# Optimization experiments

Hardware: AMD Instinct MI355X
Metric: run time of the kernel (lower is better)

The kernel has to match this reference:

```python
import jax, jax.numpy as jnp
import numpy as np

B, S, HID = 1, 1536, 6144
NH = 64           # num attention heads
DN = 128          # qk_nope_head_dim
DR = 64           # qk_rope_head_dim
DV = 128          # v_head_dim
QL = 1536         # q_lora_rank
KVL = 512         # kv_lora_rank
EPS = 1e-6
SM_SCALE = (DN + DR) ** -0.5            # qk_head_dim ** -0.5
SCALE_Q = (HID / QL) ** 0.5             # mla_scale_q_lora
SCALE_KV = (HID / KVL) ** 0.5           # mla_scale_kv_lora
ROPE_THETA = 10000.0


def rms_norm(x, w):
    xf = x.astype(jnp.float32)
    var = jnp.mean(xf * xf, axis=-1, keepdims=True)
    return (w * (xf * jax.lax.rsqrt(var + EPS))).astype(x.dtype)


def rotate_half(x):
    x1, x2 = jnp.split(x, 2, axis=-1)
    return jnp.concatenate([-x2, x1], axis=-1)


def setup_inputs() -> dict:
    key = jax.random.key(0)
    ks = jax.random.split(key, 8)
    hidden_states = jax.random.normal(ks[0], (B, S, HID), jnp.float32) * 0.02
    # rotary embeddings for the decoupled rope slice (dim DR)
    pos = jnp.arange(S, dtype=jnp.float32)
    inv_freq = 1.0 / (ROPE_THETA ** (jnp.arange(0, DR, 2, dtype=jnp.float32) / DR))
    freqs = pos[:, None] * inv_freq[None, :]          # [S, DR/2]
    emb = jnp.concatenate([freqs, freqs], axis=-1)    # [S, DR]
    cos, sin = jnp.cos(emb), jnp.sin(emb)
    w_qa = jax.random.normal(ks[1], (HID, QL), jnp.float32) / np.sqrt(HID)
    qa_ln_w = jnp.ones((QL,), jnp.float32)
    w_qb = jax.random.normal(ks[2], (QL, NH * (DN + DR)), jnp.float32) / np.sqrt(QL)
    w_kva = jax.random.normal(ks[3], (HID, KVL + DR), jnp.float32) / np.sqrt(HID)
    kva_ln_w = jnp.ones((KVL,), jnp.float32)
    # weight-absorbed kv_b_proj split: w_k [H, DN, KVL], w_v [H, KVL, DV]
    w_k = jax.random.normal(ks[4], (NH, DN, KVL), jnp.float32) / np.sqrt(KVL)
    w_v = jax.random.normal(ks[5], (NH, KVL, DV), jnp.float32) / np.sqrt(KVL)
    w_o = jax.random.normal(ks[6], (NH * DV, HID), jnp.float32) / np.sqrt(NH * DV)
    return {"hidden_states": hidden_states, "cos": cos, "sin": sin,
            "w_qa": w_qa, "qa_ln_w": qa_ln_w, "w_qb": w_qb,
            "w_kva": w_kva, "kva_ln_w": kva_ln_w,
            "w_k": w_k, "w_v": w_v, "w_o": w_o}


def reference(hidden_states, cos, sin, w_qa, qa_ln_w, w_qb, w_kva, kva_ln_w, w_k, w_v, w_o):
    b, s, _ = hidden_states.shape
    # --- Q path: low-rank compression + norm + scale + up-projection ---
    q_lat = rms_norm(hidden_states @ w_qa, qa_ln_w) * SCALE_Q        # [b,s,QL]
    q = (q_lat @ w_qb).reshape(b, s, NH, DN + DR)                    # [b,s,H,192]
    q_nope, q_pe = q[..., :DN], q[..., DN:]
    # --- KV path: compressed latent + decoupled rope key (MQA, 1 kv head) ---
    latent = hidden_states @ w_kva                                   # [b,s,KVL+DR]
    c_kv = rms_norm(latent[..., :KVL], kva_ln_w) * SCALE_KV          # [b,s,KVL]
    k_pe = latent[..., KVL:]                                         # [b,s,DR]
    # --- decoupled RoPE on rope slices only ---
    c4, s4 = cos[None, :, None, :], sin[None, :, None, :]
    q_pe = q_pe * c4 + rotate_half(q_pe) * s4                        # [b,s,H,DR]
    k_pe = k_pe * cos[None] + rotate_half(k_pe) * sin[None]          # [b,s,DR]
    # --- weight absorption: project q_nope into latent space via w_k ---
    q_abs = jnp.einsum('bshd,hdc->bshc', q_nope, w_k)                # [b,s,H,KVL]
    scores = (jnp.einsum('bshc,btc->bhst', q_abs, c_kv)
              + jnp.einsum('bshr,btr->bhst', q_pe, k_pe)) * SM_SCALE # [b,H,s,s]
    causal = jnp.tril(jnp.ones((s, s), bool))
    scores = jnp.where(causal[None, None], scores, jnp.finfo(scores.dtype).min)
    attn = jax.nn.softmax(scores, axis=-1)
    ctx = jnp.einsum('bhst,btc->bshc', attn, c_kv)                   # [b,s,H,KVL]
    out = jnp.einsum('bshc,hcd->bshd', ctx, w_v)                     # [b,s,H,DV]
    return out.reshape(b, s, NH * DV) @ w_o                          # [b,s,HID]
```

## Files before the change

### kernel.cpp

```cpp
#include <hip/hip_runtime.h>

using u16 = unsigned short;
typedef __bf16 bf16x8 __attribute__((ext_vector_type(8)));
typedef float f32x4 __attribute__((ext_vector_type(4)));

static constexpr int S = 1536;
static constexpr int HID = 6144;
static constexpr int NH = 64;
static constexpr int DN = 128;
static constexpr int DR = 64;
static constexpr int QL = 1536;
static constexpr int KVL = 512;
static constexpr float EPS = 1e-6f;
static constexpr float SM_SCALE = 0.07216878364870323f;
static constexpr float SCALE_Q = 2.0f;
static constexpr float SCALE_KV = 3.4641016151377544f;
static constexpr unsigned F32_ONE = 0x3F800000u;

__device__ inline float b2f(u16 x) {
    return __builtin_bit_cast(float, (unsigned)(((unsigned)x) << 16));
}
__device__ inline u16 f2b(float f) {
    __bf16 h = (__bf16)f;
    return __builtin_bit_cast(u16, h);
}
__device__ inline void storeC(float* p, float v) { *p = v; }
__device__ inline void storeC(u16* p, float v) { *p = f2b(v); }

typedef __attribute__((address_space(1))) void GV;
typedef __attribute__((address_space(3))) void LV;
__device__ inline void gload16(const u16* g, u16* l) {
    __builtin_amdgcn_global_load_lds((GV*)g, (LV*)l, 16, 0, 0);
}

__global__ __launch_bounds__(256)
void cvt_bf16(const void* __restrict__ src, u16* __restrict__ dst, long n,
              const unsigned* __restrict__ probe)
{
    const bool f32 = (*probe == F32_ONE);
    long i = ((long)blockIdx.x * 256 + threadIdx.x) * 8;
    if (i >= n) return;
    if (f32) {
        const float* s = (const float*)src + i;
        float4 a = *(const float4*)s;
        float4 b = *(const float4*)(s + 4);
        u16 t[8] = { f2b(a.x), f2b(a.y), f2b(a.z), f2b(a.w),
                     f2b(b.x), f2b(b.y), f2b(b.z), f2b(b.w) };
        *(uint4*)(dst + i) = *(uint4*)t;
    } else {
        *(uint4*)(dst + i) = *(const uint4*)((const u16*)src + i);
    }
}

__global__ __launch_bounds__(256)
void out_final(const u16* __restrict__ t, void* __restrict__ out, long n,
               const unsigned* __restrict__ probe)
{
    const bool f32 = (*probe == F32_ONE);
    long i = ((long)blockIdx.x * 256 + threadIdx.x) * 8;
    if (i >= n) return;
    uint4 v = *(const uint4*)(t + i);
    const u16* p = (const u16*)&v;
    if (f32) {
        float* o = (float*)out + i;
        #pragma unroll
        for (int j = 0; j < 8; ++j) o[j] = b2f(p[j]);
    } else {
        *(uint4*)((u16*)out + i) = v;
    }
}

__global__ __launch_bounds__(256)
void tconv(const void* __restrict__ src, long sBatch, int ldS,
           u16* __restrict__ dst, long dBatch, int ldD,
           const unsigned* __restrict__ probe)
{
    __shared__ u16 t[64][72];
    const bool f32 = (probe != nullptr) && (*probe == F32_ONE);
    const int r0 = blockIdx.y * 64;
    const int c0 = blockIdx.x * 64;
    const int tid = threadIdx.x;
    const int rr = tid >> 2;
    const int cc = (tid & 3) * 16;

    if (f32) {
        const float* s = (const float*)src + (long)blockIdx.z * sBatch
                       + (long)(r0 + rr) * ldS + (c0 + cc);
        u16 tmp[16];
        #pragma unroll
        for (int k = 0; k < 4; ++k) {
            float4 v = *(const float4*)(s + 4 * k);
            tmp[4*k+0] = f2b(v.x); tmp[4*k+1] = f2b(v.y);
            tmp[4*k+2] = f2b(v.z); tmp[4*k+3] = f2b(v.w);
        }
        *(uint4*)&t[rr][cc]     = *(uint4*)&tmp[0];
        *(uint4*)&t[rr][cc + 8] = *(uint4*)&tmp[8];
    } else {
        const u16* s = (const u16*)src + (long)blockIdx.z * sBatch
                     + (long)(r0 + rr) * ldS + (c0 + cc);
        *(uint4*)&t[rr][cc]     = *(const uint4*)s;
        *(uint4*)&t[rr][cc + 8] = *(const uint4*)(s + 8);
    }
    __syncthreads();
    u16 o[16];
    #pragma unroll
    for (int j = 0; j < 16; ++j) o[j] = t[cc + j][rr];
    u16* d = dst + (long)blockIdx.z * dBatch + (long)(c0 + rr) * ldD + (r0 + cc);
    *(uint4*)d       = *(uint4*)&o[0];
    *(uint4*)(d + 8) = *(uint4*)&o[8];
}

template <typename OutT>
__global__ __launch_bounds__(256)
void gemm_bt(const u16* __restrict__ A, long aB, int lda,
             const u16* __restrict__ B, long bB, int ldb,
             OutT* __restrict__ C, long cB, int ldc,
             int K, int Nvalid, int causal)
{
    const long m0 = (long)blockIdx.y * 128;
    const long n0 = (long)blockIdx.x * 128;
    if (causal == 1 && n0 >= m0 + 128) return;

    int Keff = K;
    if (causal == 2) { long kl = m0 + 128; Keff = (kl < K) ? (int)kl : K; }

    __shared__ __align__(16) u16 As[128 * 32];
    __shared__ __align__(16) u16 Bs[128 * 32];

    const int tid = threadIdx.x;
    const int lane = tid & 63, wave = tid >> 6;
    const int wm = wave >> 1, wn = wave & 1;
    const int quad = lane >> 4, r16 = lane & 15;

    A += (long)blockIdx.z * aB;
    B += (long)blockIdx.z * bB;
    C += (long)blockIdx.z * cB;

    const int srow = tid >> 2;
    const int scol = (tid & 3) * 8;

    const u16* aP  = A + (m0 + srow) * (long)lda + scol;
    const u16* aP2 = aP + 64 * (long)lda;
    const u16* bP  = B + (n0 + srow) * (long)ldb + scol;
    const u16* bP2 = bP + 64 * (long)ldb;
    u16* lA = As + srow * 32 + scol;
    u16* lB = Bs + srow * 32 + scol;

    f32x4 acc[4][4] = {};

    for (int k0 = 0; k0 < Keff; k0 += 32) {
        __syncthreads();
        gload16(aP  + k0, lA);
        gload16(aP2 + k0, lA + 64 * 32);
        gload16(bP  + k0, lB);
        gload16(bP2 + k0, lB + 64 * 32);
        asm volatile("s_waitcnt vmcnt(0)" ::: "memory");
        __syncthreads();

        bf16x8 af[4], bfr[4];
        #pragma unroll
        for (int i = 0; i < 4; ++i)
            af[i] = *(const bf16x8*)&As[(wm * 64 + i * 16 + r16) * 32 + quad * 8];
        #pragma unroll
        for (int j = 0; j < 4; ++j)
            bfr[j] = *(const bf16x8*)&Bs[(wn * 64 + j * 16 + r16) * 32 + quad * 8];
        #pragma unroll
        for (int i = 0; i < 4; ++i) {
            #pragma unroll
            for (int j = 0; j < 4; ++j)
                acc[i][j] = __builtin_amdgcn_mfma_f32_16x16x32_bf16(af[i], bfr[j], acc[i][j], 0, 0, 0);
        }
    }

    #pragma unroll
    for (int i = 0; i < 4; ++i) {
        long r = m0 + wm * 64 + i * 16 + quad * 4;
        #pragma unroll
        for (int j = 0; j < 4; ++j) {
            int c = (int)n0 + wn * 64 + j * 16 + r16;
            if (c < Nvalid) {
                #pragma unroll
                for (int g = 0; g < 4; ++g)
                    storeC(&C[(r + g) * (long)ldc + c], acc[i][j][g]);
            }
        }
    }
}

__global__ __launch_bounds__(256)
void gemm_bt_sk(const u16* __restrict__ A, int lda,
                const u16* __restrict__ B, int ldb,
                float* __restrict__ C, long cPlane, int ldc,
                int kSeg, int Nvalid)
{
    const long m0 = (long)blockIdx.y * 128;
    const long n0 = (long)blockIdx.x * 128;
    const long kBase = (long)blockIdx.z * kSeg;

    __shared__ __align__(16) u16 As[128 * 32];
    __shared__ __align__(16) u16 Bs[128 * 32];

    const int tid = threadIdx.x;
    const int lane = tid & 63, wave = tid >> 6;
    const int wm = wave >> 1, wn = wave & 1;
    const int quad = lane >> 4, r16 = lane & 15;

    const int srow = tid >> 2;
    const int scol = (tid & 3) * 8;

    const u16* aP  = A + (m0 + srow) * (long)lda + kBase + scol;
    const u16* aP2 = aP + 64 * (long)lda;
    const u16* bP  = B + (n0 + srow) * (long)ldb + kBase + scol;
    const u16* bP2 = bP + 64 * (long)ldb;
    u16* lA = As + srow * 32 + scol;
    u16* lB = Bs + srow * 32 + scol;

    f32x4 acc[4][4] = {};

    for (int k0 = 0; k0 < kSeg; k0 += 32) {
        __syncthreads();
        gload16(aP  + k0, lA);
        gload16(aP2 + k0, lA + 64 * 32);
        gload16(bP  + k0, lB);
        gload16(bP2 + k0, lB + 64 * 32);
        asm volatile("s_waitcnt vmcnt(0)" ::: "memory");
        __syncthreads();

        bf16x8 af[4], bfr[4];
        #pragma unroll
        for (int i = 0; i < 4; ++i)
            af[i] = *(const bf16x8*)&As[(wm * 64 + i * 16 + r16) * 32 + quad * 8];
        #pragma unroll
        for (int j = 0; j < 4; ++j)
            bfr[j] = *(const bf16x8*)&Bs[(wn * 64 + j * 16 + r16) * 32 + quad * 8];
        #pragma unroll
        for (int i = 0; i < 4; ++i) {
            #pragma unroll
            for (int j = 0; j < 4; ++j)
                acc[i][j] = __builtin_amdgcn_mfma_f32_16x16x32_bf16(af[i], bfr[j], acc[i][j], 0, 0, 0);
        }
    }

    float* Cz = C + (long)blockIdx.z * cPlane;
    #pragma unroll
    for (int i = 0; i < 4; ++i) {
        long r = m0 + wm * 64 + i * 16 + quad * 4;
        #pragma unroll
        for (int j = 0; j < 4; ++j) {
            int c = (int)n0 + wn * 64 + j * 16 + r16;
            if (c < Nvalid) {
                #pragma unroll
                for (int g = 0; g < 4; ++g)
                    Cz[(r + g) * (long)ldc + c] = acc[i][j][g];
            }
        }
    }
}

__global__ __launch_bounds__(256)
void sk_reduce(const float* __restrict__ parts, long n, long plane, int nsplit,
               void* __restrict__ out, int mode, const unsigned* __restrict__ probe)
{
    long i = ((long)blockIdx.x * 256 + threadIdx.x) * 4;
    if (i >= n) return;
    float4 s = *(const float4*)(parts + i);
    for (int p = 1; p < nsplit; ++p) {
        float4 v = *(const float4*)(parts + (long)p * plane + i);
        s.x += v.x; s.y += v.y; s.z += v.z; s.w += v.w;
    }
    const bool f32o = (mode == 0) || (*probe == F32_ONE);
    if (f32o) {
        *(float4*)((float*)out + i) = s;
    } else {
        u16 t[4] = { f2b(s.x), f2b(s.y), f2b(s.z), f2b(s.w) };
        *(uint2*)((u16*)out + i) = *(uint2*)t;
    }
}

__device__ inline float blockReduce(float v, bool isMax) {
    __shared__ float tmp[4];
    #pragma unroll
    for (int o = 32; o > 0; o >>= 1) {
        float ov = __shfl_down(v, o, 64);
        v = isMax ? fmaxf(v, ov) : v + ov;
    }
    int lane = threadIdx.x & 63, w = threadIdx.x >> 6;
    __syncthreads();
    if (lane == 0) tmp[w] = v;
    __syncthreads();
    v = tmp[0];
    #pragma unroll
    for (int i = 1; i < 4; ++i) v = isMax ? fmaxf(v, tmp[i]) : v + tmp[i];
    return v;
}

__global__ __launch_bounds__(256)
void qa_norm(const float* __restrict__ x, const u16* __restrict__ w, u16* __restrict__ out)
{
    int s = blockIdx.x;
    const float* row = x + (long)s * QL;
    float ss = 0.f;
    for (int c = threadIdx.x; c < QL; c += 256) { float v = row[c]; ss += v * v; }
    ss = blockReduce(ss, false);
    float inv = rsqrtf(ss / QL + EPS) * SCALE_Q;
    for (int c = threadIdx.x; c < QL; c += 256)
        out[(long)s * QL + c] = f2b(b2f(w[c]) * row[c] * inv);
}

__global__ __launch_bounds__(256)
void kva_norm_rope(const float* __restrict__ latent, const u16* __restrict__ w,
                   const u16* __restrict__ cosb, const u16* __restrict__ sinb,
                   u16* __restrict__ ckv)
{
    int s = blockIdx.x;
    const float* row = latent + (long)s * 576;
    float ss = 0.f;
    for (int c = threadIdx.x; c < KVL; c += 256) { float v = row[c]; ss += v * v; }
    ss = blockReduce(ss, false);
    float inv = rsqrtf(ss / KVL + EPS) * SCALE_KV;
    for (int c = threadIdx.x; c < KVL; c += 256)
        ckv[(long)s * 576 + c] = f2b(b2f(w[c]) * row[c] * inv);
    if (threadIdx.x < 64) {
        int d = threadIdx.x;
        float x = row[KVL + d];
        float other = (d < 32) ? -row[KVL + d + 32] : row[KVL + d - 32];
        float cv = b2f(cosb[s * 64 + d]), sv = b2f(sinb[s * 64 + d]);
        ckv[(long)s * 576 + KVL + d] = f2b(x * cv + other * sv);
    }
}

__global__ void rope_q(const u16* __restrict__ q, const u16* __restrict__ cosb,
                       const u16* __restrict__ sinb, u16* __restrict__ qcat, int h0)
{
    int s = blockIdx.x, z = blockIdx.y, d = threadIdx.x;
    const u16* qp = q + (long)s * 12288 + (h0 + z) * 192 + 128;
    float x = b2f(qp[d]);
    float other = (d < 32) ? -b2f(qp[d + 32]) : b2f(qp[d - 32]);
    float cv = b2f(cosb[s * 64 + d]), sv = b2f(sinb[s * 64 + d]);
    qcat[(long)z * (S * 576) + (long)s * 576 + 512 + d] = f2b(x * cv + other * sv);
}

__global__ __launch_bounds__(256)
void softmax_causal(float* __restrict__ scores)
{
    int s = blockIdx.x, z = blockIdx.y;
    float* row = scores + (long)z * S * S + (long)s * S;
    u16* prow = (u16*)row;
    int n = s + 1;
    float vloc[6];
    float m = -1e30f;
    #pragma unroll
    for (int i = 0; i < 6; ++i) {
        int t = threadIdx.x + i * 256;
        float v = (t < n) ? row[t] * SM_SCALE : -1e30f;
        vloc[i] = v;
        m = fmaxf(m, v);
    }
    m = blockReduce(m, true);
    float l = 0.f;
    #pragma unroll
    for (int i = 0; i < 6; ++i) {
        int t = threadIdx.x + i * 256;
        float e = (t < n) ? __expf(vloc[i] - m) : 0.f;
        vloc[i] = e;
        l += e;
    }
    l = blockReduce(l, false);
    float rinv = 1.f / l;
    #pragma unroll
    for (int i = 0; i < 6; ++i) {
        int t = threadIdx.x + i * 256;
        prow[t] = f2b(vloc[i] * rinv);
    }
}

extern "C" void kernel_launch(void* const* d_in, const int* in_sizes, int n_in,
                              void* d_out, int out_size, void* d_ws, size_t ws_size,
                              hipStream_t stream)
{
    (void)in_sizes; (void)n_in; (void)out_size;
    const unsigned* probe = (const unsigned*)d_in[4];

    const long nHid = (long)S * HID, nCos = (long)S * 64;
    const long nWqa = (long)HID * QL, nQln = QL;
    const long nWqb = (long)QL * 12288, nKln = KVL;
    const long nWk = (long)NH * DN * KVL, nWv = (long)NH * KVL * DN;
    const long nWo = (long)NH * DN * HID;

    char* ws = (char*)d_ws;
    size_t off = 0;
    auto a16 = [&](long n) { u16* p = (u16*)(ws + off); off += (size_t)n * 2; return p; };
    auto a32 = [&](long n) { float* p = (float*)(ws + off); off += (size_t)n * 4; return p; };

    u16* hid_b  = a16(nHid);
    u16* cos_b  = a16(nCos);
    u16* sin_b  = a16(nCos);
    u16* wqaT   = a16(nWqa);
    u16* qln_b  = a16(nQln);
    u16* wqbT   = a16(nWqb);
    u16* wkvaT  = a16(640L * HID);
    u16* kln_b  = a16(nKln);
    u16* wkT    = a16(nWk);
    u16* wvT    = a16(nWv);
    u16* woT    = a16(nWo);
    u16* ckvT   = a16((long)KVL * S);

    float* qlatr = a32((long)S * QL);
    float* latent = qlatr;
    u16* q_lat   = a16((long)S * QL);
    u16* qbuf    = a16((long)S * 12288);
    u16* ckv     = a16((long)S * 576);
    u16* ctxv    = a16((long)S * 8192);

    const size_t ctxAllB = (size_t)NH * S * KVL * 2;
    const size_t skOutB  = 2ul * (size_t)S * HID * 4;
    auto chunkB = [](int c) {
        return (size_t)c * S * 576 * 2 + (size_t)c * S * S * 4;
    };
    int C = 0;
    const int cand[4] = { 8, 4, 2, 1 };
    for (int ci = 0; ci < 4; ++ci) {
        size_t R = chunkB(cand[ci]); if (R < skOutB) R = skOutB;
        if (off + ctxAllB + R <= ws_size) { C = cand[ci]; break; }
    }

    auto cvt = [&](const void* s, u16* d, long n) {
        cvt_bf16<<<dim3((unsigned)((n / 8 + 255) / 256)), 256, 0, stream>>>(s, d, n, probe);
    };
    cvt(d_in[0], hid_b, nHid);
    cvt(d_in[1], cos_b, nCos);
    cvt(d_in[2], sin_b, nCos);
    cvt(d_in[4], qln_b, nQln);
    cvt(d_in[7], kln_b, nKln);

    tconv<<<dim3(24, 96, 1), 256, 0, stream>>>(d_in[3], 0, QL, wqaT, 0, HID, probe);
    tconv<<<dim3(192, 24, 1), 256, 0, stream>>>(d_in[5], 0, 12288, wqbT, 0, QL, probe);
    tconv<<<dim3(9, 96, 1), 256, 0, stream>>>(d_in[6], 0, 576, wkvaT, 0, HID, probe);
    tconv<<<dim3(8, 2, NH), 256, 0, stream>>>(d_in[8], (long)DN * KVL, KVL, wkT, (long)DN * KVL, DN, probe);
    tconv<<<dim3(2, 8, NH), 256, 0, stream>>>(d_in[9], (long)DN * KVL, DN, wvT, (long)DN * KVL, KVL, probe);
    tconv<<<dim3(96, 128, 1), 256, 0, stream>>>(d_in[10], 0, HID, woT, 0, 8192, probe);

    if (C > 0) {
        u16* ctxAll = a16((long)NH * S * KVL);
        char* Rbase = ws + off;
        float* skP   = (float*)Rbase;
        u16* qcat    = (u16*)Rbase;
        float* scores = (float*)(Rbase + (size_t)C * S * 576 * 2);

        auto rgrid = [](long n) { return dim3((unsigned)((n / 4 + 255) / 256)); };

        gemm_bt_sk<<<dim3(12, 12, 4), 256, 0, stream>>>(hid_b, HID, wqaT, HID,
                                                        skP, (long)S * QL, QL, HID / 4, QL);
        sk_reduce<<<rgrid((long)S * QL), 256, 0, stream>>>(skP, (long)S * QL, (long)S * QL, 4,
                                                           qlatr, 0, probe);
        qa_norm<<<S, 256, 0, stream>>>(qlatr, qln_b, q_lat);
        gemm_bt<u16><<<dim3(96, 12, 1), 256, 0, stream>>>(q_lat, 0, QL, wqbT, 0, QL,
                                                          qbuf, 0, 12288, QL, 12288, 0);
        gemm_bt_sk<<<dim3(5, 12, 8), 256, 0, stream>>>(hid_b, HID, wkvaT, HID,
                                                       skP, (long)S * 576, 576, HID / 8, 576);
        sk_reduce<<<rgrid((long)S * 576), 256, 0, stream>>>(skP, (long)S * 576, (long)S * 576, 8,
                                                            latent, 0, probe);
        kva_norm_rope<<<S, 256, 0, stream>>>(latent, kln_b, cos_b, sin_b, ckv);
        tconv<<<dim3(8, 24, 1), 256, 0, stream>>>(ckv, 0, 576, ckvT, 0, S, nullptr);

        for (int ch = 0; ch < NH / C; ++ch) {
            int h0 = ch * C;
            gemm_bt<u16><<<dim3(4, 12, C), 256, 0, stream>>>(
                qbuf + h0 * 192, 192, 12288, wkT + (size_t)h0 * 65536, 65536, DN,
                qcat, (long)S * 576, 576, DN, KVL, 0);
            rope_q<<<dim3(S, C), 64, 0, stream>>>(qbuf, cos_b, sin_b, qcat, h0);
            gemm_bt<float><<<dim3(12, 12, C), 256, 0, stream>>>(
                qcat, (long)S * 576, 576, ckv, 0, 576,
                scores, (long)S * S, S, 576, S, 1);
            softmax_causal<<<dim3(S, C), 256, 0, stream>>>(scores);
            gemm_bt<u16><<<dim3(4, 12, C), 256, 0, stream>>>(
                (const u16*)scores, (long)S * S * 2, 3072, ckvT, 0, S,
                ctxAll + (size_t)h0 * S * KVL, (long)S * KVL, KVL, S, KVL, 2);
        }
        gemm_bt<u16><<<dim3(1, 12, NH), 256, 0, stream>>>(
            ctxAll, (long)S * KVL, KVL, wvT, 65536, KVL,
            ctxv, 128, 8192, KVL, DN, 0);
        gemm_bt_sk<<<dim3(48, 12, 2), 256, 0, stream>>>(ctxv, 8192, woT, 8192,
                                                        skP, (long)S * HID, HID, 8192 / 2, HID);
        sk_reduce<<<rgrid(nHid), 256, 0, stream>>>(skP, nHid, nHid, 2, d_out, 2, probe);
    } else {
        const size_t perHB = (size_t)S * 576 * 2 + (size_t)S * S * 4 + (size_t)S * KVL * 2;
        int Cf = 1;
        if      (off + 8 * perHB <= ws_size) Cf = 8;
        else if (off + 4 * perHB <= ws_size) Cf = 4;
        else if (off + 2 * perHB <= ws_size) Cf = 2;

        u16* qcat    = a16((long)Cf * S * 576);
        float* scores = a32((long)Cf * S * S);
        u16* ctx     = a16((long)Cf * S * KVL);
        u16* outTmp  = wqaT;

        gemm_bt<float><<<dim3(12, 12, 1), 256, 0, stream>>>(hid_b, 0, HID, wqaT, 0, HID,
                                                            qlatr, 0, QL, HID, QL, 0);
        qa_norm<<<S, 256, 0, stream>>>(qlatr, qln_b, q_lat);
        gemm_bt<u16><<<dim3(96, 12, 1), 256, 0, stream>>>(q_lat, 0, QL, wqbT, 0, QL,
                                                          qbuf, 0, 12288, QL, 12288, 0);
        gemm_bt<float><<<dim3(5, 12, 1), 256, 0, stream>>>(hid_b, 0, HID, wkvaT, 0, HID,
                                                           latent, 0, 576, HID, 576, 0);
        kva_norm_rope<<<S, 256, 0, stream>>>(latent, kln_b, cos_b, sin_b, ckv);
        tconv<<<dim3(8, 24, 1), 256, 0, stream>>>(ckv, 0, 576, ckvT, 0, S, nullptr);

        for (int ch = 0; ch < NH / Cf; ++ch) {
            int h0 = ch * Cf;
            gemm_bt<u16><<<dim3(4, 12, Cf), 256, 0, stream>>>(
                qbuf + h0 * 192, 192, 12288, wkT + (size_t)h0 * 65536, 65536, DN,
                qcat, (long)S * 576, 576, DN, KVL, 0);
            rope_q<<<dim3(S, Cf), 64, 0, stream>>>(qbuf, cos_b, sin_b, qcat, h0);
            gemm_bt<float><<<dim3(12, 12, Cf), 256, 0, stream>>>(
                qcat, (long)S * 576, 576, ckv, 0, 576,
                scores, (long)S * S, S, 576, S, 1);
            softmax_causal<<<dim3(S, Cf), 256, 0, stream>>>(scores);
            gemm_bt<u16><<<dim3(4, 12, Cf), 256, 0, stream>>>(
                (const u16*)scores, (long)S * S * 2, 3072, ckvT, 0, S,
                ctx, (long)S * KVL, KVL, S, KVL, 2);
            gemm_bt<u16><<<dim3(1, 12, Cf), 256, 0, stream>>>(
                ctx, (long)S * KVL, KVL, wvT + (size_t)h0 * 65536, 65536, KVL,
                ctxv + h0 * 128, 128, 8192, KVL, DN, 0);
        }
        gemm_bt<u16><<<dim3(48, 12, 1), 256, 0, stream>>>(ctxv, 0, 8192, woT, 0, 8192,
                                                          outTmp, 0, HID, 8192, HID, 0);
        out_final<<<dim3((unsigned)((nHid / 8 + 255) / 256)), 256, 0, stream>>>(
            outTmp, d_out, nHid, probe);
    }
}
```

Before: 1.820 ms.

## Double GEMM K-tile with XOR-swizzled LDS, XCD-aware block remap, larger head chunks

Both GEMM kernels now stage a 64-wide K slice per iteration instead of 32, and run two MFMA sub-steps per barrier pair. Global loads are XOR-swizzled into the LDS rows to avoid bank conflicts on the fragment reads. A new xcd_remap reorders workgroups so that neighbouring output tiles land on the same XCD, for better L2 reuse; it is enabled for the large projection GEMMs and always for split-K. The attention head-chunk candidates now go up to 64 heads when the workspace allows, cutting launch count. The cost is twice the LDS per block and more index arithmetic, which may lower occupancy.

```diff
diff --git a/kernel.cpp b/kernel.cpp
--- a/kernel.cpp
+++ b/kernel.cpp
@@ -110,65 +110,85 @@
     *(uint4*)(d + 8) = *(uint4*)&o[8];
 }
 
+__device__ inline void xcd_remap(int& bx, int& by, int gx, int gy)
+{
+    const int nwg = gx * gy;
+    const int L = by * gx + bx;
+    const int q = nwg >> 3, r = nwg & 7;
+    const int xcd = L & 7, i = L >> 3;
+    const int d = ((xcd < r) ? xcd * (q + 1) : r * (q + 1) + (xcd - r) * q) + i;
+    bx = d / gy;  by = d - bx * gy;
+}
+
 template <typename OutT>
 __global__ __launch_bounds__(256)
 void gemm_bt(const u16* __restrict__ A, long aB, int lda,
              const u16* __restrict__ B, long bB, int ldb,
              OutT* __restrict__ C, long cB, int ldc,
-             int K, int Nvalid, int causal)
-{
-    const long m0 = (long)blockIdx.y * 128;
-    const long n0 = (long)blockIdx.x * 128;
+             int K, int Nvalid, int causal, int swz)
+{
+    int bx = blockIdx.x, by = blockIdx.y;
+    if (swz) xcd_remap(bx, by, gridDim.x, gridDim.y);
+    const long m0 = (long)by * 128;
+    const long n0 = (long)bx * 128;
     if (causal == 1 && n0 >= m0 + 128) return;
 
     int Keff = K;
     if (causal == 2) { long kl = m0 + 128; Keff = (kl < K) ? (int)kl : K; }
 
-    __shared__ __align__(16) u16 As[128 * 32];
-    __shared__ __align__(16) u16 Bs[128 * 32];
+    __shared__ __align__(16) u16 As[128 * 64];
+    __shared__ __align__(16) u16 Bs[128 * 64];
 
     const int tid = threadIdx.x;
     const int lane = tid & 63, wave = tid >> 6;
     const int wm = wave >> 1, wn = wave & 1;
     const int quad = lane >> 4, r16 = lane & 15;
+    const int rx = r16 & 7;
 
     A += (long)blockIdx.z * aB;
     B += (long)blockIdx.z * bB;
     C += (long)blockIdx.z * cB;
 
-    const int srow = tid >> 2;
-    const int scol = (tid & 3) * 8;
-
-    const u16* aP  = A + (m0 + srow) * (long)lda + scol;
-    const u16* aP2 = aP + 64 * (long)lda;
-    const u16* bP  = B + (n0 + srow) * (long)ldb + scol;
-    const u16* bP2 = bP + 64 * (long)ldb;
-    u16* lA = As + srow * 32 + scol;
-    u16* lB = Bs + srow * 32 + scol;
+    const int srow = tid >> 3;
+    const int gck = ((tid & 7) ^ (srow & 7)) * 8;
+
+    const u16* aP = A + (m0 + srow) * (long)lda + gck;
+    const u16* bP = B + (n0 + srow) * (long)ldb + gck;
+    u16* lA = As + tid * 8;
+    u16* lB = Bs + tid * 8;
+    const long l32a = 32 * (long)lda, l32b = 32 * (long)ldb;
 
     f32x4 acc[4][4] = {};
 
-    for (int k0 = 0; k0 < Keff; k0 += 32) {
+    for (int k0 = 0; k0 < Keff; k0 += 64) {
         __syncthreads();
-        gload16(aP  + k0, lA);
-        gload16(aP2 + k0, lA + 64 * 32);
-        gload16(bP  + k0, lB);
-        gload16(bP2 + k0, lB + 64 * 32);
+        gload16(aP + k0,            lA);
+        gload16(aP + l32a + k0,     lA + 2048);
+        gload16(aP + 2 * l32a + k0, lA + 4096);
+        gload16(aP + 3 * l32a + k0, lA + 6144);
+        gload16(bP + k0,            lB);
+        gload16(bP + l32b + k0,     lB + 2048);
+        gload16(bP + 2 * l32b + k0, lB + 4096);
+        gload16(bP + 3 * l32b + k0, lB + 6144);
         asm volatile("s_waitcnt vmcnt(0)" ::: "memory");
         __syncthreads();
 
-        bf16x8 af[4], bfr[4];
         #pragma unroll
-        for (int i = 0; i < 4; ++i)
-            af[i] = *(const bf16x8*)&As[(wm * 64 + i * 16 + r16) * 32 + quad * 8];
-        #pragma unroll
-        for (int j = 0; j < 4; ++j)
-            bfr[j] = *(const bf16x8*)&Bs[(wn * 64 + j * 16 + r16) * 32 + quad * 8];
-        #pragma unroll
-        for (int i = 0; i < 4; ++i) {
+        for (int kk = 0; kk < 2; ++kk) {
+            bf16x8 af[4], bfr[4];
+            const int ck = ((kk * 4 + quad) ^ rx) * 8;
+            #pragma unroll
+            for (int i = 0; i < 4; ++i)
+                af[i] = *(const bf16x8*)&As[(wm * 64 + i * 16 + r16) * 64 + ck];
             #pragma unroll
             for (int j = 0; j < 4; ++j)
-                acc[i][j] = __builtin_amdgcn_mfma_f32_16x16x32_bf16(af[i], bfr[j], acc[i][j], 0, 0, 0);
+                bfr[j] = *(const bf16x8*)&Bs[(wn * 64 + j * 16 + r16) * 64 + ck];
+            #pragma unroll
+            for (int i = 0; i < 4; ++i) {
+                #pragma unroll
+                for (int j = 0; j < 4; ++j)
+                    acc[i][j] = __builtin_amdgcn_mfma_f32_16x16x32_bf16(af[i], bfr[j], acc[i][j], 0, 0, 0);
+            }
         }
     }
 
@@ -193,51 +213,61 @@
                 float* __restrict__ C, long cPlane, int ldc,
                 int kSeg, int Nvalid)
 {
-    const long m0 = (long)blockIdx.y * 128;
-    const long n0 = (long)blockIdx.x * 128;
+    int bx = blockIdx.x, by = blockIdx.y;
+    xcd_remap(bx, by, gridDim.x, gridDim.y);
+    const long m0 = (long)by * 128;
+    const long n0 = (long)bx * 128;
     const long kBase = (long)blockIdx.z * kSeg;
 
-    __shared__ __align__(16) u16 As[128 * 32];
-    __shared__ __align__(16) u16 Bs[128 * 32];
+    __shared__ __align__(16) u16 As[128 * 64];
+    __shared__ __align__(16) u16 Bs[128 * 64];
 
     const int tid = threadIdx.x;
     const int lane = tid & 63, wave = tid >> 6;
     const int wm = wave >> 1, wn = wave & 1;
     const int quad = lane >> 4, r16 = lane & 15;
-
-    const int srow = tid >> 2;
-    const int scol = (tid & 3) * 8;
-
-    const u16* aP  = A + (m0 + srow) * (long)lda + kBase + scol;
-    const u16* aP2 = aP + 64 * (long)lda;
-    const u16* bP  = B + (n0 + srow) * (long)ldb + kBase + scol;
-    const u16* bP2 = bP + 64 * (long)ldb;
-    u16* lA = As + srow * 32 + scol;
-    u16* lB = Bs + srow * 32 + scol;
+    const int rx = r16 & 7;
+
+    const int srow = tid >> 3;
+    const int gck = ((tid & 7) ^ (srow & 7)) * 8;
+
+    const u16* aP = A + (m0 + srow) * (long)lda + kBase + gck;
+    const u16* bP = B + (n0 + srow) * (long)ldb + kBase + gck;
+    u16* lA = As + tid * 8;
+    u16* lB = Bs + tid * 8;
+    const long l32a = 32 * (long)lda, l32b = 32 * (long)ldb;
 
     f32x4 acc[4][4] = {};
 
-    for (int k0 = 0; k0 < kSeg; k0 += 32) {
+    for (int k0 = 0; k0 < kSeg; k0 += 64) {
         __syncthreads();
-        gload16(aP  + k0, lA);
-        gload16(aP2 + k0, lA + 64 * 32);
-        gload16(bP  + k0, lB);
-        gload16(bP2 + k0, lB + 64 * 32);
+        gload16(aP + k0,            lA);
+        gload16(aP + l32a + k0,     lA + 2048);
+        gload16(aP + 2 * l32a + k0, lA + 4096);
+        gload16(aP + 3 * l32a + k0, lA + 6144);
+        gload16(bP + k0,            lB);
+        gload16(bP + l32b + k0,     lB + 2048);
+        gload16(bP + 2 * l32b + k0, lB + 4096);
+        gload16(bP + 3 * l32b + k0, lB + 6144);
         asm volatile("s_waitcnt vmcnt(0)" ::: "memory");
         __syncthreads();
 
-        bf16x8 af[4], bfr[4];
         #pragma unroll
-        for (int i = 0; i < 4; ++i)
-            af[i] = *(const bf16x8*)&As[(wm * 64 + i * 16 + r16) * 32 + quad * 8];
-        #pragma unroll
-        for (int j = 0; j < 4; ++j)
-            bfr[j] = *(const bf16x8*)&Bs[(wn * 64 + j * 16 + r16) * 32 + quad * 8];
-        #pragma unroll
-        for (int i = 0; i < 4; ++i) {
+        for (int kk = 0; kk < 2; ++kk) {
+            bf16x8 af[4], bfr[4];
+            const int ck = ((kk * 4 + quad) ^ rx) * 8;
+            #pragma unroll
+            for (int i = 0; i < 4; ++i)
+                af[i] = *(const bf16x8*)&As[(wm * 64 + i * 16 + r16) * 64 + ck];
             #pragma unroll
             for (int j = 0; j < 4; ++j)
-                acc[i][j] = __builtin_amdgcn_mfma_f32_16x16x32_bf16(af[i], bfr[j], acc[i][j], 0, 0, 0);
+                bfr[j] = *(const bf16x8*)&Bs[(wn * 64 + j * 16 + r16) * 64 + ck];
+            #pragma unroll
+            for (int i = 0; i < 4; ++i) {
+                #pragma unroll
+                for (int j = 0; j < 4; ++j)
+                    acc[i][j] = __builtin_amdgcn_mfma_f32_16x16x32_bf16(af[i], bfr[j], acc[i][j], 0, 0, 0);
+            }
         }
     }
 
@@ -418,8 +448,8 @@
         return (size_t)c * S * 576 * 2 + (size_t)c * S * S * 4;
     };
     int C = 0;
-    const int cand[4] = { 8, 4, 2, 1 };
-    for (int ci = 0; ci < 4; ++ci) {
+    const int cand[7] = { 64, 32, 16, 8, 4, 2, 1 };
+    for (int ci = 0; ci < 7; ++ci) {
         size_t R = chunkB(cand[ci]); if (R < skOutB) R = skOutB;
         if (off + ctxAllB + R <= ws_size) { C = cand[ci]; break; }
     }
@@ -455,7 +485,7 @@
                                                            qlatr, 0, probe);
         qa_norm<<<S, 256, 0, stream>>>(qlatr, qln_b, q_lat);
         gemm_bt<u16><<<dim3(96, 12, 1), 256, 0, stream>>>(q_lat, 0, QL, wqbT, 0, QL,
-                                                          qbuf, 0, 12288, QL, 12288, 0);
+                                                          qbuf, 0, 12288, QL, 12288, 0, 1);
         gemm_bt_sk<<<dim3(5, 12, 8), 256, 0, stream>>>(hid_b, HID, wkvaT, HID,
                                                        skP, (long)S * 576, 576, HID / 8, 576);
         sk_reduce<<<rgrid((long)S * 576), 256, 0, stream>>>(skP, (long)S * 576, (long)S * 576, 8,
@@ -467,19 +497,19 @@
             int h0 = ch * C;
             gemm_bt<u16><<<dim3(4, 12, C), 256, 0, stream>>>(
                 qbuf + h0 * 192, 192, 12288, wkT + (size_t)h0 * 65536, 65536, DN,
-                qcat, (long)S * 576, 576, DN, KVL, 0);
+                qcat, (long)S * 576, 576, DN, KVL, 0, 0);
             rope_q<<<dim3(S, C), 64, 0, stream>>>(qbuf, cos_b, sin_b, qcat, h0);
             gemm_bt<float><<<dim3(12, 12, C), 256, 0, stream>>>(
                 qcat, (long)S * 576, 576, ckv, 0, 576,
-                scores, (long)S * S, S, 576, S, 1);
+                scores, (long)S * S, S, 576, S, 1, 0);
             softmax_causal<<<dim3(S, C), 256, 0, stream>>>(scores);
             gemm_bt<u16><<<dim3(4, 12, C), 256, 0, stream>>>(
                 (const u16*)scores, (long)S * S * 2, 3072, ckvT, 0, S,
-                ctxAll + (size_t)h0 * S * KVL, (long)S * KVL, KVL, S, KVL, 2);
+                ctxAll + (size_t)h0 * S * KVL, (long)S * KVL, KVL, S, KVL, 2, 0);
         }
         gemm_bt<u16><<<dim3(1, 12, NH), 256, 0, stream>>>(
             ctxAll, (long)S * KVL, KVL, wvT, 65536, KVL,
-            ctxv, 128, 8192, KVL, DN, 0);
+            ctxv, 128, 8192, KVL, DN, 0, 0);
         gemm_bt_sk<<<dim3(48, 12, 2), 256, 0, stream>>>(ctxv, 8192, woT, 8192,
                                                         skP, (long)S * HID, HID, 8192 / 2, HID);
         sk_reduce<<<rgrid(nHid), 256, 0, stream>>>(skP, nHid, nHid, 2, d_out, 2, probe);
@@ -496,12 +526,12 @@
         u16* outTmp  = wqaT;
 
         gemm_bt<float><<<dim3(12, 12, 1), 256, 0, stream>>>(hid_b, 0, HID, wqaT, 0, HID,
-                                                            qlatr, 0, QL, HID, QL, 0);
+                                                            qlatr, 0, QL, HID, QL, 0, 1);
         qa_norm<<<S, 256, 0, stream>>>(qlatr, qln_b, q_lat);
         gemm_bt<u16><<<dim3(96, 12, 1), 256, 0, stream>>>(q_lat, 0, QL, wqbT, 0, QL,
-                                                          qbuf, 0, 12288, QL, 12288, 0);
+                                                          qbuf, 0, 12288, QL, 12288, 0, 1);
         gemm_bt<float><<<dim3(5, 12, 1), 256, 0, stream>>>(hid_b, 0, HID, wkvaT, 0, HID,
-                                                           latent, 0, 576, HID, 576, 0);
+                                                           latent, 0, 576, HID, 576, 0, 1);
         kva_norm_rope<<<S, 256, 0, stream>>>(latent, kln_b, cos_b, sin_b, ckv);
         tconv<<<dim3(8, 24, 1), 256, 0, stream>>>(ckv, 0, 576, ckvT, 0, S, nullptr);
 
@@ -509,21 +539,21 @@
             int h0 = ch * Cf;
             gemm_bt<u16><<<dim3(4, 12, Cf), 256, 0, stream>>>(
                 qbuf + h0 * 192, 192, 12288, wkT + (size_t)h0 * 65536, 65536, DN,
-                qcat, (long)S * 576, 576, DN, KVL, 0);
+                qcat, (long)S * 576, 576, DN, KVL, 0, 0);
             rope_q<<<dim3(S, Cf), 64, 0, stream>>>(qbuf, cos_b, sin_b, qcat, h0);
             gemm_bt<float><<<dim3(12, 12, Cf), 256, 0, stream>>>(
                 qcat, (long)S * 576, 576, ckv, 0, 576,
-                scores, (long)S * S, S, 576, S, 1);
+                scores, (long)S * S, S, 576, S, 1, 0);
             softmax_causal<<<dim3(S, Cf), 256, 0, stream>>>(scores);
             gemm_bt<u16><<<dim3(4, 12, Cf), 256, 0, stream>>>(
                 (const u16*)scores, (long)S * S * 2, 3072, ckvT, 0, S,
-                ctx, (long)S * KVL, KVL, S, KVL, 2);
+                ctx, (long)S * KVL, KVL, S, KVL, 2, 0);
             gemm_bt<u16><<<dim3(1, 12, Cf), 256, 0, stream>>>(
                 ctx, (long)S * KVL, KVL, wvT + (size_t)h0 * 65536, 65536, KVL,
-                ctxv + h0 * 128, 128, 8192, KVL, DN, 0);
+                ctxv + h0 * 128, 128, 8192, KVL, DN, 0, 0);
         }
         gemm_bt<u16><<<dim3(48, 12, 1), 256, 0, stream>>>(ctxv, 0, 8192, woT, 0, 8192,
-                                                          outTmp, 0, HID, 8192, HID, 0);
+                                                          outTmp, 0, HID, 8192, HID, 0, 1);
         out_final<<<dim3((unsigned)((nHid / 8 + 255) / 256)), 256, 0, stream>>>(
             outTmp, d_out, nHid, probe);
     }
```

Result: faster. 1.603 ms (-11.9%).
